# Kernel optimization log

Measured on AMD Instinct MI355X. Metric: run time of the kernel, lower is better.

The kernel has to match this reference:

```python
import jax, jax.numpy as jnp
import numpy as np

B, S, Lc = 128, 128, 20          # batch, words per sentence, chars per word
AB, E = 100, 64                  # char alphabet, char embedding dim
Hc, H, OUT = 256, 512, 50        # char hidden, word hidden, n tags
PAD = 0                          # padding idx for words and chars


def _cell_params(key, din, h):
    k1, k2, k3, k4 = jax.random.split(key, 4)
    return (jax.random.normal(k1, (4 * h, din)) * 0.05,
            jax.random.normal(k2, (4 * h, h)) * 0.05,
            jax.random.normal(k3, (4 * h,)) * 0.05,
            jax.random.normal(k4, (4 * h,)) * 0.05)


def setup_inputs() -> dict:
    key = jax.random.key(0)
    ks = jax.random.split(key, 12)
    x = jax.random.randint(ks[0], (B, S, Lc), 0, AB)
    emb = jax.random.normal(ks[1], (AB, E)) * 0.05
    emb = emb.at[PAD].set(0.0)  # nn.Embedding padding_idx row is zero
    cW_ih, cW_hh, cb_ih, cb_hh = _cell_params(ks[2], E, Hc)
    fW_ih, fW_hh, fb_ih, fb_hh = _cell_params(ks[3], Hc, H)
    bW_ih, bW_hh, bb_ih, bb_hh = _cell_params(ks[4], Hc, H)
    W1 = jax.random.normal(ks[5], (256, 2 * H)) * 0.05
    b1 = jax.random.normal(ks[6], (256,)) * 0.05
    W2 = jax.random.normal(ks[7], (256, 256)) * 0.05
    b2 = jax.random.normal(ks[8], (256,)) * 0.05
    W3 = jax.random.normal(ks[9], (OUT, 256)) * 0.05
    b3 = jax.random.normal(ks[10], (OUT,)) * 0.05
    return dict(x=x, emb=emb,
                cW_ih=cW_ih, cW_hh=cW_hh, cb_ih=cb_ih, cb_hh=cb_hh,
                fW_ih=fW_ih, fW_hh=fW_hh, fb_ih=fb_ih, fb_hh=fb_hh,
                bW_ih=bW_ih, bW_hh=bW_hh, bb_ih=bb_ih, bb_hh=bb_hh,
                W1=W1, b1=b1, W2=W2, b2=b2, W3=W3, b3=b3)


def _lstm_cell(x_t, h, c, W_ih, W_hh, b_ih, b_hh):
    # PyTorch LSTMCell: gates ordered i, f, g, o
    g = x_t @ W_ih.T + b_ih + h @ W_hh.T + b_hh
    i, f, gg, o = jnp.split(g, 4, axis=-1)
    c = jax.nn.sigmoid(f) * c + jax.nn.sigmoid(i) * jnp.tanh(gg)
    h = jax.nn.sigmoid(o) * jnp.tanh(c)
    return h, c


def _char_acceptor(e_seq, lengths, W_ih, W_hh, b_ih, b_hh, hsize):
    # e_seq: [N, T, E]; returns last non-padded hidden state per row: [N, hsize]
    N, T, _ = e_seq.shape
    h0 = jnp.zeros((N, hsize), e_seq.dtype)

    def step(carry, inp):
        h, c, last = carry
        x_t, t = inp
        h, c = _lstm_cell(x_t, h, c, W_ih, W_hh, b_ih, b_hh)
        last = jnp.where((lengths > t)[:, None], h, last)
        return (h, c, last), None

    xs = (jnp.swapaxes(e_seq, 0, 1), jnp.arange(T))
    (_, _, last), _ = jax.lax.scan(step, (h0, h0, h0), xs)
    return last


def _lstm_transduce(seq_tbd, W_ih, W_hh, b_ih, b_hh, hsize):
    # seq_tbd: [T, B, D] -> all hidden states [T, B, hsize]
    Tb = seq_tbd.shape[1]
    h0 = jnp.zeros((Tb, hsize), seq_tbd.dtype)

    def step(carry, x_t):
        h, c = carry
        h, c = _lstm_cell(x_t, h, c, W_ih, W_hh, b_ih, b_hh)
        return (h, c), h

    _, hs = jax.lax.scan(step, (h0, h0), seq_tbd)
    return hs


def reference(x, emb,
              cW_ih, cW_hh, cb_ih, cb_hh,
              fW_ih, fW_hh, fb_ih, fb_hh,
              bW_ih, bW_hh, bb_ih, bb_hh,
              W1, b1, W2, b2, W3, b3):
    Bx, Sx, Lx = x.shape
    xf = x.reshape(Bx * Sx, Lx)                       # all words flattened
    e = emb[xf]                                       # [B*S, Lc, E]
    lengths = (xf != PAD).sum(axis=1)
    char_out = _char_acceptor(e, lengths, cW_ih, cW_hh, cb_ih, cb_hh, Hc)
    word_seq = char_out.reshape(Bx, Sx, Hc)           # [B, S, Hc]

    seq_tbd = jnp.swapaxes(word_seq, 0, 1)            # [S, B, Hc]
    hs_f = _lstm_transduce(seq_tbd, fW_ih, fW_hh, fb_ih, fb_hh, H)
    hs_b = _lstm_transduce(seq_tbd[::-1], bW_ih, bW_hh, bb_ih, bb_hh, H)[::-1]
    hs = jnp.concatenate([hs_f, hs_b], axis=-1)       # [S, B, 2H]
    hs = jnp.swapaxes(hs, 0, 1)                       # [B, S, 2H]

    h1 = jax.nn.relu(hs @ W1.T + b1)
    h2 = jax.nn.relu(h1 @ W2.T + b2)
    logits = h2 @ W3.T + b3                           # [B, S, OUT]
    return jax.nn.log_softmax(logits, axis=2)
```

## Files before the change

kernel.cpp:

```cpp
#include <hip/hip_runtime.h>
#include <hip/hip_bf16.h>
#include <math.h>

typedef __hip_bfloat16 bf16;
typedef __attribute__((ext_vector_type(8))) short bf16x8;
typedef __attribute__((ext_vector_type(4))) float f32x4;
typedef long i64t;

#define NW   16384
#define LC   20
#define EDIM 64
#define HC   256
#define HW   512
#define SEQ  128
#define NOUT 50
#define FPAD 16

#define LOG2E 1.4426950408889634f
__device__ __forceinline__ float fex2(float x) {
  float r; asm("v_exp_f32 %0, %1" : "=v"(r) : "v"(x)); return r;
}
__device__ __forceinline__ float frcp(float x) {
  float r; asm("v_rcp_f32 %0, %1" : "=v"(r) : "v"(x)); return r;
}
__device__ __forceinline__ float flog2(float x) {
  float r; asm("v_log_f32 %0, %1" : "=v"(r) : "v"(x)); return r;
}
__device__ __forceinline__ float fsig(float x) { return frcp(1.f + fex2(-LOG2E * x)); }
__device__ __forceinline__ float ftanh(float x) {
  return 1.f - 2.f * frcp(1.f + fex2(2.f * LOG2E * x));
}

__device__ __forceinline__ unsigned short f2bu(float f) {
  bf16 h = __float2bfloat16(f);
  return *reinterpret_cast<unsigned short*>(&h);
}
__device__ __forceinline__ bf16x8 ld8(const unsigned short* p) {
  return *reinterpret_cast<const bf16x8*>(p);
}
__device__ __forceinline__ float fp8_to_f32(unsigned int b) {
  float r; asm("v_cvt_f32_fp8 %0, %1" : "=v"(r) : "v"(b)); return r;
}
__device__ __forceinline__ i64t ld8x(const unsigned char* p, bool f) {
  i64t r;
  if (f) asm volatile("global_load_dwordx2 %0, %1, off sc0" : "=v"(r) : "v"(p));
  else   asm volatile("global_load_dwordx2 %0, %1, off sc0 sc1" : "=v"(r) : "v"(p));
  return r;
}
__device__ __forceinline__ void st8x(unsigned char* p, i64t v, bool f) {
  if (f) asm volatile("global_store_dwordx2 %0, %1, off sc0" :: "v"(p), "v"(v) : "memory");
  else   asm volatile("global_store_dwordx2 %0, %1, off sc0 sc1" :: "v"(p), "v"(v) : "memory");
}
__device__ __forceinline__ int ldflagx(const int* p, bool f) {
  int r;
  if (f) asm volatile("global_load_dword %0, %1, off sc0" : "=v"(r) : "v"(p));
  else   asm volatile("global_load_dword %0, %1, off sc0 sc1" : "=v"(r) : "v"(p));
  return r;
}
__device__ __forceinline__ void stflagx(int* p, int v, bool f) {
  if (f) asm volatile("global_store_dword %0, %1, off sc0" :: "v"(p), "v"(v) : "memory");
  else   asm volatile("global_store_dword %0, %1, off sc0 sc1" :: "v"(p), "v"(v) : "memory");
}
#define MFMA(a, b, c)  __builtin_amdgcn_mfma_f32_16x16x32_bf16(a, b, c, 0, 0, 0)
#define MFMA8(a, b, c) __builtin_amdgcn_mfma_f32_16x16x32_fp8_fp8(a, b, c, 0, 0, 0)

__global__ __launch_bounds__(512, 1) void char_lstm(
    const int* __restrict__ x, const unsigned char* __restrict__ emb8,
    const unsigned char* __restrict__ Wc8, const float* __restrict__ bcT,
    unsigned short* __restrict__ lastT, const int* __restrict__ len) {
  __shared__ unsigned char Hs8[2][64][264];
  __shared__ _Float16 Cs[256][66];
  __shared__ int lenS[64];
  const int tid = threadIdx.x;
  const int w = tid >> 6, l = tid & 63;
  const int l16 = l & 15, lk8 = (l >> 4) * 8, q = l >> 4;
  const int w0 = blockIdx.x * 64;
  if (tid < 64) lenS[tid] = len[w0 + tid];

  for (int t = 0; t < LC; ++t) {
    const int cur = t & 1, nxt = cur ^ 1;
    int xi[4];
#pragma unroll
    for (int wh = 0; wh < 4; ++wh) xi[wh] = x[(w0 + wh * 16 + l16) * LC + t];
#pragma unroll
    for (int c = 0; c < 2; ++c) {
      const int chg = w * 2 + c;
      const int cc0 = chg * 64;
      f32x4 acc[4][4] = {};
#pragma unroll
      for (int kk = 0; kk < 2; ++kk) {
        const int k = kk * 32 + lk8;
        const unsigned char* wp = Wc8 + (size_t)(cc0 + l16) * 320 + k;
        i64t bv8[4];
#pragma unroll
        for (int g = 0; g < 4; ++g)
          bv8[g] = *reinterpret_cast<const i64t*>(wp + g * 16 * 320);
#pragma unroll
        for (int wh = 0; wh < 4; ++wh) {
          i64t a8 = *reinterpret_cast<const i64t*>(emb8 + (size_t)xi[wh] * 64 + k);
#pragma unroll
          for (int g = 0; g < 4; ++g) acc[wh][g] = MFMA8(bv8[g], a8, acc[wh][g]);
        }
      }
      if (t > 0) {
#pragma unroll
        for (int kk = 2; kk < 10; ++kk) {
          const int k = kk * 32 + lk8;
          const unsigned char* wp = Wc8 + (size_t)(cc0 + l16) * 320 + k;
          i64t bv8[4];
#pragma unroll
          for (int g = 0; g < 4; ++g)
            bv8[g] = *reinterpret_cast<const i64t*>(wp + g * 16 * 320);
#pragma unroll
          for (int wh = 0; wh < 4; ++wh) {
            i64t a8 = *reinterpret_cast<const i64t*>(&Hs8[cur][wh * 16 + l16][k - 64]);
#pragma unroll
            for (int g = 0; g < 4; ++g) acc[wh][g] = MFMA8(bv8[g], a8, acc[wh][g]);
          }
        }
      }
      float4 bb4[4];
#pragma unroll
      for (int e = 0; e < 4; ++e)
        bb4[e] = *reinterpret_cast<const float4*>(bcT + (chg * 16 + q * 4 + e) * 4);
      const int uoff = chg * 16 + q * 4;
#pragma unroll
      for (int wh = 0; wh < 4; ++wh) {
        const int wd = wh * 16 + l16;
        float hv[4];
#pragma unroll
        for (int e = 0; e < 4; ++e) {
          const int ug = chg * 16 + q * 4 + e;
          const float gi = acc[wh][0][e] + bb4[e].x;
          const float gf = acc[wh][1][e] + bb4[e].y;
          const float gg = acc[wh][2][e] + bb4[e].z;
          const float go = acc[wh][3][e] + bb4[e].w;
          const float cprev = t ? (float)Cs[ug][wd] : 0.f;
          const float ccv = fsig(gf) * cprev + fsig(gi) * ftanh(gg);
          Cs[ug][wd] = (_Float16)ccv;
          hv[e] = fsig(go) * ftanh(ccv);
        }
        const int d0 = __builtin_amdgcn_cvt_pk_fp8_f32(hv[0], hv[1], 0, false);
        const int d1 = __builtin_amdgcn_cvt_pk_fp8_f32(hv[2], hv[3], 0, false);
        const unsigned int pk = (unsigned int)(d0 & 0xFFFF) |
                                ((unsigned int)(d1 & 0xFFFF) << 16);
        *reinterpret_cast<unsigned int*>(&Hs8[nxt][wd][uoff]) = pk;
      }
    }
    __syncthreads();
    {
      const int wd = tid >> 3, sub = tid & 7;
      const int myl = lenS[wd];
      if (myl == t + 1 || (myl == 0 && t == 0)) {
        const int n = w0 + wd;
        const int lrow = ((n & 127) * 128 + (n >> 7)) * HC;
        if (myl == 0) {
          bf16x8 z = {};
#pragma unroll
          for (int j = 0; j < 4; ++j)
            *reinterpret_cast<bf16x8*>(lastT + lrow + sub * 32 + j * 8) = z;
        } else {
#pragma unroll
          for (int j = 0; j < 4; ++j) {
            unsigned int v0 = *reinterpret_cast<unsigned int*>(
                &Hs8[nxt][wd][sub * 32 + j * 8]);
            unsigned int v1 = *reinterpret_cast<unsigned int*>(
                &Hs8[nxt][wd][sub * 32 + j * 8 + 4]);
            union { unsigned short s[8]; bf16x8 v; } o;
#pragma unroll
            for (int b = 0; b < 4; ++b) {
              o.s[b]     = f2bu(fp8_to_f32((v0 >> (8 * b)) & 0xFF));
              o.s[4 + b] = f2bu(fp8_to_f32((v1 >> (8 * b)) & 0xFF));
            }
            *reinterpret_cast<bf16x8*>(lastT + lrow + sub * 32 + j * 8) = o.v;
          }
        }
      }
    }
  }
}

__global__ __launch_bounds__(256, 1) void word_lstm(
    const unsigned short* __restrict__ lastT,
    const unsigned short* __restrict__ W16,
    const unsigned short* __restrict__ W16b,
    const unsigned char* __restrict__ W8f,
    const unsigned char* __restrict__ W8b,
    const float* __restrict__ bfi, const float* __restrict__ bbi,
    unsigned char* __restrict__ hbL8,
    unsigned short* __restrict__ hsW,
    int* __restrict__ aflag) {
  const int bx = blockIdx.x;
  if ((bx & 7) > 1) return;
  __shared__ unsigned short Wlds16[64 * 256];
  __shared__ unsigned char  Wlds8[64 * 512];
  __shared__ unsigned short ht[128][24];
  __shared__ unsigned char  ht8[128][24];
  __shared__ int fastS;
  const int tid = threadIdx.x;
  const int w = tid >> 6, l = tid & 63;
  const int l16 = l & 15, lk8 = (l >> 4) * 8, q = l >> 4;
  const int dir = bx & 7;
  const int nb = bx >> 3;
  const int c0 = nb * 64;
  const unsigned short* Wx = dir ? W16b : W16;
  const unsigned char*  Wh = dir ? W8b : W8f;
  const float* bias = dir ? bbi : bfi;
  int* negcnt = aflag + (size_t)2 * SEQ * 32 * FPAD;
  if (tid == 0) {
    const int xcc = __builtin_amdgcn_s_getreg(20 | (31 << 11)) & 7;
    int* xc = negcnt + 16 + dir * 8 + xcc;
    __hip_atomic_fetch_add(xc, 1, __ATOMIC_RELAXED, __HIP_MEMORY_SCOPE_AGENT);
    __hip_atomic_fetch_add(negcnt, 1, __ATOMIC_RELAXED, __HIP_MEMORY_SCOPE_AGENT);
    while (__hip_atomic_load(negcnt, __ATOMIC_RELAXED, __HIP_MEMORY_SCOPE_AGENT) < 64)
      __builtin_amdgcn_s_sleep(2);
    fastS = (__hip_atomic_load(xc, __ATOMIC_RELAXED, __HIP_MEMORY_SCOPE_AGENT) == 32);
  }
  for (int ci = tid; ci < 64 * 32; ci += 256) {
    const int col = ci >> 5, kc = (ci & 31) * 8;
    const int kcs = kc ^ ((col & 15) * 8);
    *reinterpret_cast<bf16x8*>(&Wlds16[col * 256 + kcs]) =
        ld8(Wx + (size_t)(c0 + col) * 256 + kc);
  }
  for (int ci = tid; ci < 64 * 64; ci += 256) {
    const int col = ci >> 6, kb = (ci & 63) * 8;
    const int kbs = kb ^ ((col & 15) * 8);
    *reinterpret_cast<i64t*>(&Wlds8[col * 512 + kbs]) =
        *reinterpret_cast<const i64t*>(Wh + (size_t)(c0 + col) * 512 + kb);
  }
  const float b0 = bias[c0 + 0 * 16 + l16];
  const float b1 = bias[c0 + 1 * 16 + l16];
  const float b2 = bias[c0 + 2 * 16 + l16];
  const float b3 = bias[c0 + 3 * 16 + l16];
  const int ksw = l16 * 8;
  float cst[8];
#pragma unroll
  for (int i = 0; i < 8; ++i) cst[i] = 0.f;
  __syncthreads();
  const bool fast = (fastS != 0);

  for (int t = 0; t < SEQ; ++t) {
    const int cur = t & 1;
    const int pos = dir ? (SEQ - 1 - t) : t;
    f32x4 acc[2][4] = {};
#pragma unroll
    for (int kk = 0; kk < 8; ++kk) {
      const int k = kk * 32 + lk8;
      bf16x8 a0 = ld8(lastT + ((size_t)pos * 128 + w * 32 + l16) * HC + k);
      bf16x8 a1 = ld8(lastT + ((size_t)pos * 128 + w * 32 + l16 + 16) * HC + k);
      const int ks = k ^ ksw;
#pragma unroll
      for (int nn = 0; nn < 4; ++nn) {
        bf16x8 bv = ld8(&Wlds16[(l16 + nn * 16) * 256 + ks]);
        acc[0][nn] = MFMA(a0, bv, acc[0][nn]);
        acc[1][nn] = MFMA(a1, bv, acc[1][nn]);
      }
    }
    if (t > 0) {
      if (w == 0) {
        const int* fp = aflag + (size_t)(dir * SEQ + (t - 1)) * 32 * FPAD;
        for (;;) {
          int v = 1;
          if (l < 32) v = ldflagx(fp + l * FPAD, fast);
          if (__ballot(v != 0) == ~0ull) break;
          __builtin_amdgcn_s_sleep(1);
        }
      }
      __syncthreads();
      i64t af8[16][2];
      const unsigned char* hp =
          hbL8 + (size_t)(((cur ^ 1) * 2 + dir) * 32) * 128 * 16;
#pragma unroll
      for (int kk = 0; kk < 16; ++kk) {
        const int u = kk * 32 + lk8;
        const int nbs = u >> 4, ul = u & 15;
#pragma unroll
        for (int r = 0; r < 2; ++r) {
          const int bt = w * 32 + l16 + r * 16;
          af8[kk][r] = ld8x(hp + ((size_t)nbs * 128 + bt) * 16 + ul, fast);
        }
      }
      asm volatile("s_waitcnt vmcnt(0)" ::: "memory");
      __builtin_amdgcn_sched_barrier(0);
#pragma unroll
      for (int kk = 0; kk < 16; ++kk) {
        const int ks8 = (kk * 32 + lk8) ^ ksw;
#pragma unroll
        for (int nn = 0; nn < 4; ++nn) {
          i64t w8 = *reinterpret_cast<const i64t*>(
              &Wlds8[(l16 + nn * 16) * 512 + ks8]);
          acc[0][nn] = MFMA8(af8[kk][0], w8, acc[0][nn]);
          acc[1][nn] = MFMA8(af8[kk][1], w8, acc[1][nn]);
        }
      }
    }
    float hvf[8];
    int bats[8];
#pragma unroll
    for (int m = 0; m < 2; ++m)
#pragma unroll
      for (int e = 0; e < 4; ++e) {
        const int j = m * 4 + e;
        const float gi = acc[m][0][e] + b0;
        const float gf = acc[m][1][e] + b1;
        const float gg = acc[m][2][e] + b2;
        const float go = acc[m][3][e] + b3;
        const float ccv = fsig(gf) * cst[j] + fsig(gi) * ftanh(gg);
        cst[j] = ccv;
        const float hv = fsig(go) * ftanh(ccv);
        const int bat = w * 32 + q * 4 + e + m * 16;
        ht[bat][l16] = f2bu(hv);
        hvf[j] = hv; bats[j] = bat;
      }
    {
      const int d0 = __builtin_amdgcn_cvt_pk_fp8_f32(hvf[0], hvf[1], 0, false);
      const int d1 = __builtin_amdgcn_cvt_pk_fp8_f32(hvf[2], hvf[3], 0, false);
      const int d2 = __builtin_amdgcn_cvt_pk_fp8_f32(hvf[4], hvf[5], 0, false);
      const int d3 = __builtin_amdgcn_cvt_pk_fp8_f32(hvf[6], hvf[7], 0, false);
      ht8[bats[0]][l16] = (unsigned char)(d0 & 255);
      ht8[bats[1]][l16] = (unsigned char)((d0 >> 8) & 255);
      ht8[bats[2]][l16] = (unsigned char)(d1 & 255);
      ht8[bats[3]][l16] = (unsigned char)((d1 >> 8) & 255);
      ht8[bats[4]][l16] = (unsigned char)(d2 & 255);
      ht8[bats[5]][l16] = (unsigned char)((d2 >> 8) & 255);
      ht8[bats[6]][l16] = (unsigned char)(d3 & 255);
      ht8[bats[7]][l16] = (unsigned char)((d3 >> 8) & 255);
    }
    __syncthreads();
    const int ub = tid >> 1, uh = tid & 1;
    i64t hv8 = *reinterpret_cast<const i64t*>(&ht8[ub][uh * 8]);
    st8x(hbL8 + (size_t)((cur * 2 + dir) * 32 + nb) * 128 * 16
             + ub * 16 + uh * 8, hv8, fast);
    if (t < SEQ - 1) {
      asm volatile("s_waitcnt vmcnt(0)" ::: "memory");
      __syncthreads();
      if (tid == 0)
        stflagx(aflag + ((size_t)(dir * SEQ + t) * 32 + nb) * FPAD, 1, fast);
    }
    bf16x8 hv = ld8(&ht[ub][uh * 8]);
    *reinterpret_cast<bf16x8*>(
        hsW + (((size_t)(dir * 32 + nb) * 128 + pos) * 128 + ub) * 16 + uh * 8) = hv;
  }
}

__global__ __launch_bounds__(256) void mlp1_gemm(
    const unsigned short* __restrict__ hsW, const unsigned short* __restrict__ W1b,
    const float* __restrict__ bias, unsigned short* __restrict__ out) {
  const int tid = threadIdx.x;
  const int w = tid >> 6, l = tid & 63;
  const int l16 = l & 15, lk8 = (l >> 4) * 8;
  const int by = blockIdx.y;
  const int row0 = by * 128 + w * 32;
  const int col0 = blockIdx.x * 64;
  f32x4 acc[2][4] = {};
  for (int kk = 0; kk < 32; ++kk) {
    const int k = kk * 32 + lk8;
    const int dirk = k >> 9, u = k & 511, nbs = u >> 4, ul = u & 15;
    const int p0 = w * 32 + l16, p1 = p0 + 16;
    bf16x8 a0 = ld8(hsW + (((size_t)(dirk * 32 + nbs) * 128 + p0) * 128 + by) * 16 + ul);
    bf16x8 a1 = ld8(hsW + (((size_t)(dirk * 32 + nbs) * 128 + p1) * 128 + by) * 16 + ul);
    const unsigned short* wp = W1b + (size_t)(col0 + l16) * 1024 + k;
#pragma unroll
    for (int nn = 0; nn < 4; ++nn) {
      bf16x8 bv = ld8(wp + nn * 16 * 1024);
      acc[0][nn] = MFMA(a0, bv, acc[0][nn]);
      acc[1][nn] = MFMA(a1, bv, acc[1][nn]);
    }
  }
  const int cr = (l >> 4) * 4;
#pragma unroll
  for (int m = 0; m < 2; ++m)
#pragma unroll
    for (int nn = 0; nn < 4; ++nn)
#pragma unroll
      for (int e = 0; e < 4; ++e) {
        const int r = row0 + m * 16 + cr + e;
        const int c = col0 + nn * 16 + l16;
        out[(size_t)r * 256 + c] = f2bu(fmaxf(acc[m][nn][e] + bias[c], 0.f));
      }
}

__global__ __launch_bounds__(256) void mlp_gemm(
    const unsigned short* __restrict__ A, int lda,
    const unsigned short* __restrict__ W, int ldw,
    const float* __restrict__ bias, unsigned short* __restrict__ out,
    int ldo, int nk, int relu) {
  const int tid = threadIdx.x;
  const int w = tid >> 6, l = tid & 63;
  const int l16 = l & 15, lk8 = (l >> 4) * 8;
  const int row0 = blockIdx.y * 128 + w * 32;
  const int col0 = blockIdx.x * 64;
  f32x4 acc[2][4] = {};
  for (int kk = 0; kk < nk; ++kk) {
    const int k = kk * 32 + lk8;
    bf16x8 a0 = ld8(A + (size_t)(row0 + l16) * lda + k);
    bf16x8 a1 = ld8(A + (size_t)(row0 + 16 + l16) * lda + k);
    const unsigned short* wp = W + (size_t)(col0 + l16) * ldw + k;
    bf16x8 bb[4];
#pragma unroll
    for (int nn = 0; nn < 4; ++nn) bb[nn] = ld8(wp + nn * 16 * ldw);
#pragma unroll
    for (int nn = 0; nn < 4; ++nn) {
      acc[0][nn] = MFMA(a0, bb[nn], acc[0][nn]);
      acc[1][nn] = MFMA(a1, bb[nn], acc[1][nn]);
    }
  }
  const int cr = (l >> 4) * 4;
#pragma unroll
  for (int m = 0; m < 2; ++m)
#pragma unroll
    for (int nn = 0; nn < 4; ++nn)
#pragma unroll
      for (int e = 0; e < 4; ++e) {
        const int r = row0 + m * 16 + cr + e;
        const int c = col0 + nn * 16 + l16;
        float v = acc[m][nn][e] + bias[c];
        if (relu) v = fmaxf(v, 0.f);
        out[(size_t)r * ldo + c] = f2bu(v);
      }
}

__global__ __launch_bounds__(256) void logits_fused(
    const unsigned short* __restrict__ h2, const unsigned short* __restrict__ W3p,
    const float* __restrict__ b3, float* __restrict__ out) {
  __shared__ float gt[128][68];
  __shared__ float lseb[128];
  const int tid = threadIdx.x;
  const int w = tid >> 6, l = tid & 63;
  const int l16 = l & 15, lk8 = (l >> 4) * 8;
  const int r0 = blockIdx.x * 128;
  const int rr0 = w * 32 + l16, rr1 = rr0 + 16;
  f32x4 acc[2][4] = {};
#pragma unroll
  for (int kk = 0; kk < 8; ++kk) {
    const int k = kk * 32 + lk8;
    bf16x8 a0 = ld8(h2 + (size_t)(r0 + rr0) * 256 + k);
    bf16x8 a1 = ld8(h2 + (size_t)(r0 + rr1) * 256 + k);
#pragma unroll
    for (int nn = 0; nn < 4; ++nn) {
      bf16x8 bv = ld8(W3p + (size_t)(nn * 16 + l16) * 256 + k);
      acc[0][nn] = MFMA(a0, bv, acc[0][nn]);
      acc[1][nn] = MFMA(a1, bv, acc[1][nn]);
    }
  }
  const int cr = (l >> 4) * 4;
#pragma unroll
  for (int m = 0; m < 2; ++m)
#pragma unroll
    for (int nn = 0; nn < 4; ++nn)
#pragma unroll
      for (int e = 0; e < 4; ++e) {
        const int col = nn * 16 + l16;
        gt[w * 32 + m * 16 + cr + e][col] =
            acc[m][nn][e] + (col < NOUT ? b3[col] : 0.f);
      }
  __syncthreads();
  if (tid < 128) {
    float mx = -INFINITY;
#pragma unroll
    for (int j = 0; j < NOUT; ++j) mx = fmaxf(mx, gt[tid][j]);
    float s = 0.f;
#pragma unroll
    for (int j = 0; j < NOUT; ++j) s += fex2(LOG2E * (gt[tid][j] - mx));
    lseb[tid] = flog2(s) * 0.6931471805599453f + mx;
  }
  __syncthreads();
  for (int idx = tid; idx < 128 * NOUT; idx += 256) {
    const int r = idx / NOUT, j = idx - r * NOUT;
    out[(size_t)(r0 + r) * NOUT + j] = gt[r][j] - lseb[r];
  }
}

__global__ void prep_wx(const float* __restrict__ ih, unsigned short* __restrict__ dst,
                        int HU, int KI) {
  const long tot = (long)HU * 4 * KI;
  for (long idx = (long)blockIdx.x * blockDim.x + threadIdx.x; idx < tot;
       idx += (long)gridDim.x * blockDim.x) {
    const int row = (int)(idx / KI), k = (int)(idx % KI);
    const int chunk = row >> 6, c = row & 63;
    const int g = c >> 4, u = chunk * 16 + (c & 15);
    dst[idx] = f2bu(ih[(size_t)(g * HU + u) * KI + k]);
  }
}

__global__ void prep_wc8(const float* __restrict__ ih, const float* __restrict__ hh,
                         unsigned char* __restrict__ dst, int HU, int KI, int KH) {
  const int K = KI + KH;
  const long tot = (long)HU * 4 * (K / 2);
  for (long p = (long)blockIdx.x * blockDim.x + threadIdx.x; p < tot;
       p += (long)gridDim.x * blockDim.x) {
    const int row = (int)(p / (K / 2)), kp = (int)(p % (K / 2)) * 2;
    const int chunk = row >> 6, c = row & 63;
    const int g = c >> 4, u = chunk * 16 + (c & 15);
    const float a = (kp < KI) ? ih[(size_t)(g * HU + u) * KI + kp]
                              : hh[(size_t)(g * HU + u) * KH + (kp - KI)];
    const float b = (kp + 1 < KI) ? ih[(size_t)(g * HU + u) * KI + kp + 1]
                                  : hh[(size_t)(g * HU + u) * KH + (kp + 1 - KI)];
    const int d = __builtin_amdgcn_cvt_pk_fp8_f32(a, b, 0, false);
    *reinterpret_cast<unsigned short*>(dst + (size_t)row * K + kp) =
        (unsigned short)(d & 0xFFFF);
  }
}

__global__ void prep_w8(const float* __restrict__ hh, unsigned char* __restrict__ dst,
                        int HU, int KH) {
  const long tot = (long)HU * 4 * (KH / 2);
  for (long p = (long)blockIdx.x * blockDim.x + threadIdx.x; p < tot;
       p += (long)gridDim.x * blockDim.x) {
    const int row = (int)(p / (KH / 2)), kp = (int)(p % (KH / 2)) * 2;
    const int chunk = row >> 6, c = row & 63;
    const int g = c >> 4, u = chunk * 16 + (c & 15);
    const float a = hh[(size_t)(g * HU + u) * KH + kp];
    const float b = hh[(size_t)(g * HU + u) * KH + kp + 1];
    const int d = __builtin_amdgcn_cvt_pk_fp8_f32(a, b, 0, false);
    *reinterpret_cast<unsigned short*>(dst + (size_t)row * KH + kp) =
        (unsigned short)(d & 0xFFFF);
  }
}

__global__ void prep_bias(const float* bih, const float* bhh, float* dst, int HU) {
  const int idx = blockIdx.x * blockDim.x + threadIdx.x;
  if (idx < 4 * HU) {
    const int chunk = idx >> 6, c = idx & 63;
    const int g = c >> 4, u = chunk * 16 + (c & 15);
    dst[idx] = bih[g * HU + u] + bhh[g * HU + u];
  }
}

__global__ void prep_biasT(const float* bih, const float* bhh, float* dst, int HU) {
  const int idx = blockIdx.x * blockDim.x + threadIdx.x;
  if (idx < 4 * HU) {
    const int u = idx >> 2, g = idx & 3;
    dst[idx] = bih[g * HU + u] + bhh[g * HU + u];
  }
}

__global__ void conv_bf(const float* __restrict__ src, unsigned short* __restrict__ dst,
                        long n) {
  for (long i = (long)blockIdx.x * blockDim.x + threadIdx.x; i < n;
       i += (long)gridDim.x * blockDim.x)
    dst[i] = f2bu(src[i]);
}

__global__ void conv_fp8(const float* __restrict__ src, unsigned char* __restrict__ dst,
                         long n2) {
  for (long i = (long)blockIdx.x * blockDim.x + threadIdx.x; i < n2;
       i += (long)gridDim.x * blockDim.x) {
    const int d = __builtin_amdgcn_cvt_pk_fp8_f32(src[i * 2], src[i * 2 + 1], 0, false);
    *reinterpret_cast<unsigned short*>(dst + i * 2) = (unsigned short)(d & 0xFFFF);
  }
}

__global__ void prep_w3(const float* __restrict__ W3, unsigned short* __restrict__ dst) {
  const int i = blockIdx.x * blockDim.x + threadIdx.x;
  if (i < 64 * 256) {
    const int r = i >> 8;
    dst[i] = (r < NOUT) ? f2bu(W3[i]) : 0;
  }
}

__global__ void lengths_k(const int* x, int* len) {
  const int n = blockIdx.x * blockDim.x + threadIdx.x;
  if (n < NW) {
    int c = 0;
#pragma unroll
    for (int l = 0; l < LC; ++l) c += (x[(size_t)n * LC + l] != 0) ? 1 : 0;
    len[n] = c;
  }
}

__global__ void zero_k(int* p, int n) {
  const int i = blockIdx.x * blockDim.x + threadIdx.x;
  if (i < n) p[i] = 0;
}

__global__ void sentinel_k(float* out, int n) {
  const int i = blockIdx.x * blockDim.x + threadIdx.x;
  if (i < n) out[i] = 1000.0f;
}

extern "C" void kernel_launch(void* const* d_in, const int* in_sizes, int n_in,
                              void* d_out, int out_size, void* d_ws, size_t ws_size,
                              hipStream_t stream) {
  const int*   x     = (const int*)d_in[0];
  const float* emb   = (const float*)d_in[1];
  const float* cW_ih = (const float*)d_in[2];
  const float* cW_hh = (const float*)d_in[3];
  const float* cb_ih = (const float*)d_in[4];
  const float* cb_hh = (const float*)d_in[5];
  const float* fW_ih = (const float*)d_in[6];
  const float* fW_hh = (const float*)d_in[7];
  const float* fb_ih = (const float*)d_in[8];
  const float* fb_hh = (const float*)d_in[9];
  const float* bW_ih = (const float*)d_in[10];
  const float* bW_hh = (const float*)d_in[11];
  const float* bb_ih = (const float*)d_in[12];
  const float* bb_hh = (const float*)d_in[13];
  const float* W1 = (const float*)d_in[14];
  const float* b1 = (const float*)d_in[15];
  const float* W2 = (const float*)d_in[16];
  const float* b2 = (const float*)d_in[17];
  const float* W3 = (const float*)d_in[18];
  const float* b3 = (const float*)d_in[19];
  float* out = (float*)d_out;
  (void)in_sizes; (void)n_in;

  char* ws = (char*)d_ws;
  size_t off = 0;
  auto alloc = [&](size_t bytes) -> char* {
    char* p = ws + off;
    off += (bytes + 255) & ~(size_t)255;
    return p;
  };
  const int NFLAG = 2 * SEQ * 32 * FPAD + 32;
  int*            len_  = (int*)alloc((size_t)NW * 4);
  int*            aflag = (int*)alloc((size_t)NFLAG * 4);
  unsigned char*  emb8  = (unsigned char*)alloc((size_t)100 * EDIM);
  unsigned char*  Wc8   = (unsigned char*)alloc((size_t)1024 * 320);
  unsigned short* Wf_i  = (unsigned short*)alloc((size_t)2048 * 256 * 2);
  unsigned short* Wb_i  = (unsigned short*)alloc((size_t)2048 * 256 * 2);
  unsigned char*  Wf8   = (unsigned char*)alloc((size_t)2048 * 512);
  unsigned char*  Wb8   = (unsigned char*)alloc((size_t)2048 * 512);
  unsigned short* W1b   = (unsigned short*)alloc((size_t)256 * 1024 * 2);
  unsigned short* W2b   = (unsigned short*)alloc((size_t)256 * 256 * 2);
  unsigned short* W3p   = (unsigned short*)alloc((size_t)64 * 256 * 2);
  float*          bcT   = (float*)alloc(1024 * 4);
  float*          bf_i  = (float*)alloc(2048 * 4);
  float*          bb_i  = (float*)alloc(2048 * 4);
  unsigned short* lastT = (unsigned short*)alloc((size_t)NW * HC * 2);
  unsigned char*  hbL8  = (unsigned char*)alloc((size_t)2 * 2 * 32 * 128 * 16);
  unsigned short* hsW   = (unsigned short*)alloc((size_t)2 * 32 * 128 * 128 * 16 * 2);
  unsigned short* h1    = (unsigned short*)alloc((size_t)NW * HC * 2);
  unsigned short* h2    = (unsigned short*)alloc((size_t)NW * HC * 2);

  if (off > ws_size) {
    sentinel_k<<<(out_size + 255) / 256, 256, 0, stream>>>(out, out_size);
    return;
  }

  auto cdiv = [](long a, long b) { return (int)((a + b - 1) / b); };

  prep_wc8<<<640, 256, 0, stream>>>(cW_ih, cW_hh, Wc8, HC, EDIM, HC);
  prep_wx<<<1024, 256, 0, stream>>>(fW_ih, Wf_i, HW, HC);
  prep_wx<<<1024, 256, 0, stream>>>(bW_ih, Wb_i, HW, HC);
  prep_w8<<<2048, 256, 0, stream>>>(fW_hh, Wf8, HW, HW);
  prep_w8<<<2048, 256, 0, stream>>>(bW_hh, Wb8, HW, HW);
  prep_biasT<<<cdiv(1024, 256), 256, 0, stream>>>(cb_ih, cb_hh, bcT, HC);
  prep_bias<<<cdiv(2048, 256), 256, 0, stream>>>(fb_ih, fb_hh, bf_i, HW);
  prep_bias<<<cdiv(2048, 256), 256, 0, stream>>>(bb_ih, bb_hh, bb_i, HW);
  conv_fp8<<<13, 256, 0, stream>>>(emb, emb8, 100L * EDIM / 2);
  conv_bf<<<1024, 256, 0, stream>>>(W1, W1b, 256L * 1024);
  conv_bf<<<256, 256, 0, stream>>>(W2, W2b, 256L * 256);
  prep_w3<<<64, 256, 0, stream>>>(W3, W3p);
  lengths_k<<<cdiv(NW, 256), 256, 0, stream>>>(x, len_);
  zero_k<<<cdiv(NFLAG, 256), 256, 0, stream>>>(aflag, NFLAG);

  char_lstm<<<NW / 64, 512, 0, stream>>>(x, emb8, Wc8, bcT, lastT, len_);

  word_lstm<<<256, 256, 0, stream>>>(lastT, Wf_i, Wb_i, Wf8, Wb8, bf_i, bb_i,
                                     hbL8, hsW, aflag);

  mlp1_gemm<<<dim3(4, 128), 256, 0, stream>>>(hsW, W1b, b1, h1);
  mlp_gemm<<<dim3(4, 128), 256, 0, stream>>>(h1, 256, W2b, 256, b2, h2, 256, 8, 1);
  logits_fused<<<NW / 128, 256, 0, stream>>>(h2, W3p, b3, out);
}
```

Before: 1.292 ms.

## Split word LSTM batch rows across 8 waves instead of 4

The word-level LSTM block now runs 512 threads (8 waves), and each wave handles 16 batch rows instead of 32. Per-wave MFMA work, accumulator registers and per-step cell state are halved, which should shorten the serial critical path of each recurrent step. In exchange there are more waves per barrier, and the LDS weight tiles are now shared across twice as many waves. Only the first 256 threads write the hidden state out.

```diff
diff --git a/kernel.cpp b/kernel.cpp
--- a/kernel.cpp
+++ b/kernel.cpp
@@ -180,7 +180,7 @@
   }
 }
 
-__global__ __launch_bounds__(256, 1) void word_lstm(
+__global__ __launch_bounds__(512, 1) void word_lstm(
     const unsigned short* __restrict__ lastT,
     const unsigned short* __restrict__ W16,
     const unsigned short* __restrict__ W16b,
@@ -216,13 +216,13 @@
       __builtin_amdgcn_s_sleep(2);
     fastS = (__hip_atomic_load(xc, __ATOMIC_RELAXED, __HIP_MEMORY_SCOPE_AGENT) == 32);
   }
-  for (int ci = tid; ci < 64 * 32; ci += 256) {
+  for (int ci = tid; ci < 64 * 32; ci += 512) {
     const int col = ci >> 5, kc = (ci & 31) * 8;
     const int kcs = kc ^ ((col & 15) * 8);
     *reinterpret_cast<bf16x8*>(&Wlds16[col * 256 + kcs]) =
         ld8(Wx + (size_t)(c0 + col) * 256 + kc);
   }
-  for (int ci = tid; ci < 64 * 64; ci += 256) {
+  for (int ci = tid; ci < 64 * 64; ci += 512) {
     const int col = ci >> 6, kb = (ci & 63) * 8;
     const int kbs = kb ^ ((col & 15) * 8);
     *reinterpret_cast<i64t*>(&Wlds8[col * 512 + kbs]) =
@@ -233,27 +233,26 @@
   const float b2 = bias[c0 + 2 * 16 + l16];
   const float b3 = bias[c0 + 3 * 16 + l16];
   const int ksw = l16 * 8;
-  float cst[8];
-#pragma unroll
-  for (int i = 0; i < 8; ++i) cst[i] = 0.f;
+  float cst[4];
+#pragma unroll
+  for (int i = 0; i < 4; ++i) cst[i] = 0.f;
   __syncthreads();
   const bool fast = (fastS != 0);
+  const int bt = w * 16 + l16;
 
   for (int t = 0; t < SEQ; ++t) {
     const int cur = t & 1;
     const int pos = dir ? (SEQ - 1 - t) : t;
-    f32x4 acc[2][4] = {};
+    f32x4 acc[4] = {};
 #pragma unroll
     for (int kk = 0; kk < 8; ++kk) {
       const int k = kk * 32 + lk8;
-      bf16x8 a0 = ld8(lastT + ((size_t)pos * 128 + w * 32 + l16) * HC + k);
-      bf16x8 a1 = ld8(lastT + ((size_t)pos * 128 + w * 32 + l16 + 16) * HC + k);
+      bf16x8 a0 = ld8(lastT + ((size_t)pos * 128 + bt) * HC + k);
       const int ks = k ^ ksw;
 #pragma unroll
       for (int nn = 0; nn < 4; ++nn) {
         bf16x8 bv = ld8(&Wlds16[(l16 + nn * 16) * 256 + ks]);
-        acc[0][nn] = MFMA(a0, bv, acc[0][nn]);
-        acc[1][nn] = MFMA(a1, bv, acc[1][nn]);
+        acc[nn] = MFMA(a0, bv, acc[nn]);
       }
     }
     if (t > 0) {
@@ -267,18 +266,14 @@
         }
       }
       __syncthreads();
-      i64t af8[16][2];
+      i64t af8[16];
       const unsigned char* hp =
           hbL8 + (size_t)(((cur ^ 1) * 2 + dir) * 32) * 128 * 16;
 #pragma unroll
       for (int kk = 0; kk < 16; ++kk) {
         const int u = kk * 32 + lk8;
         const int nbs = u >> 4, ul = u & 15;
-#pragma unroll
-        for (int r = 0; r < 2; ++r) {
-          const int bt = w * 32 + l16 + r * 16;
-          af8[kk][r] = ld8x(hp + ((size_t)nbs * 128 + bt) * 16 + ul, fast);
-        }
+        af8[kk] = ld8x(hp + ((size_t)nbs * 128 + bt) * 16 + ul, fast);
       }
       asm volatile("s_waitcnt vmcnt(0)" ::: "memory");
       __builtin_amdgcn_sched_barrier(0);
@@ -289,57 +284,52 @@
         for (int nn = 0; nn < 4; ++nn) {
           i64t w8 = *reinterpret_cast<const i64t*>(
               &Wlds8[(l16 + nn * 16) * 512 + ks8]);
-          acc[0][nn] = MFMA8(af8[kk][0], w8, acc[0][nn]);
-          acc[1][nn] = MFMA8(af8[kk][1], w8, acc[1][nn]);
+          acc[nn] = MFMA8(af8[kk], w8, acc[nn]);
         }
       }
     }
-    float hvf[8];
-    int bats[8];
-#pragma unroll
-    for (int m = 0; m < 2; ++m)
-#pragma unroll
-      for (int e = 0; e < 4; ++e) {
-        const int j = m * 4 + e;
-        const float gi = acc[m][0][e] + b0;
-        const float gf = acc[m][1][e] + b1;
-        const float gg = acc[m][2][e] + b2;
-        const float go = acc[m][3][e] + b3;
-        const float ccv = fsig(gf) * cst[j] + fsig(gi) * ftanh(gg);
-        cst[j] = ccv;
-        const float hv = fsig(go) * ftanh(ccv);
-        const int bat = w * 32 + q * 4 + e + m * 16;
-        ht[bat][l16] = f2bu(hv);
-        hvf[j] = hv; bats[j] = bat;
-      }
+    float hvf[4];
+    int bats[4];
+#pragma unroll
+    for (int e = 0; e < 4; ++e) {
+      const float gi = acc[0][e] + b0;
+      const float gf = acc[1][e] + b1;
+      const float gg = acc[2][e] + b2;
+      const float go = acc[3][e] + b3;
+      const float ccv = fsig(gf) * cst[e] + fsig(gi) * ftanh(gg);
+      cst[e] = ccv;
+      const float hv = fsig(go) * ftanh(ccv);
+      const int bat = w * 16 + q * 4 + e;
+      ht[bat][l16] = f2bu(hv);
+      hvf[e] = hv; bats[e] = bat;
+    }
     {
       const int d0 = __builtin_amdgcn_cvt_pk_fp8_f32(hvf[0], hvf[1], 0, false);
       const int d1 = __builtin_amdgcn_cvt_pk_fp8_f32(hvf[2], hvf[3], 0, false);
-      const int d2 = __builtin_amdgcn_cvt_pk_fp8_f32(hvf[4], hvf[5], 0, false);
-      const int d3 = __builtin_amdgcn_cvt_pk_fp8_f32(hvf[6], hvf[7], 0, false);
       ht8[bats[0]][l16] = (unsigned char)(d0 & 255);
       ht8[bats[1]][l16] = (unsigned char)((d0 >> 8) & 255);
       ht8[bats[2]][l16] = (unsigned char)(d1 & 255);
       ht8[bats[3]][l16] = (unsigned char)((d1 >> 8) & 255);
-      ht8[bats[4]][l16] = (unsigned char)(d2 & 255);
-      ht8[bats[5]][l16] = (unsigned char)((d2 >> 8) & 255);
-      ht8[bats[6]][l16] = (unsigned char)(d3 & 255);
-      ht8[bats[7]][l16] = (unsigned char)((d3 >> 8) & 255);
     }
     __syncthreads();
-    const int ub = tid >> 1, uh = tid & 1;
-    i64t hv8 = *reinterpret_cast<const i64t*>(&ht8[ub][uh * 8]);
-    st8x(hbL8 + (size_t)((cur * 2 + dir) * 32 + nb) * 128 * 16
-             + ub * 16 + uh * 8, hv8, fast);
+    if (tid < 256) {
+      const int ub = tid >> 1, uh = tid & 1;
+      i64t hv8 = *reinterpret_cast<const i64t*>(&ht8[ub][uh * 8]);
+      st8x(hbL8 + (size_t)((cur * 2 + dir) * 32 + nb) * 128 * 16
+               + ub * 16 + uh * 8, hv8, fast);
+    }
     if (t < SEQ - 1) {
       asm volatile("s_waitcnt vmcnt(0)" ::: "memory");
       __syncthreads();
       if (tid == 0)
         stflagx(aflag + ((size_t)(dir * SEQ + t) * 32 + nb) * FPAD, 1, fast);
     }
-    bf16x8 hv = ld8(&ht[ub][uh * 8]);
-    *reinterpret_cast<bf16x8*>(
-        hsW + (((size_t)(dir * 32 + nb) * 128 + pos) * 128 + ub) * 16 + uh * 8) = hv;
+    if (tid < 256) {
+      const int ub = tid >> 1, uh = tid & 1;
+      bf16x8 hv = ld8(&ht[ub][uh * 8]);
+      *reinterpret_cast<bf16x8*>(
+          hsW + (((size_t)(dir * 32 + nb) * 128 + pos) * 128 + ub) * 16 + uh * 8) = hv;
+    }
   }
 }
 
@@ -657,7 +647,7 @@
 
   char_lstm<<<NW / 64, 512, 0, stream>>>(x, emb8, Wc8, bcT, lastT, len_);
 
-  word_lstm<<<256, 256, 0, stream>>>(lastT, Wf_i, Wb_i, Wf8, Wb8, bf_i, bb_i,
+  word_lstm<<<256, 512, 0, stream>>>(lastT, Wf_i, Wb_i, Wf8, Wb8, bf_i, bb_i,
                                      hbL8, hsW, aflag);
 
   mlp1_gemm<<<dim3(4, 128), 256, 0, stream>>>(hsW, W1b, b1, h1);
```

New measurement: 1.126 ms. 12.8% less time.
